# Kernel optimization log

Hardware: AMD Instinct MI355X
Metric: run time of the kernel (lower is better)

Reference implementation:

```python
import jax, jax.numpy as jnp
import numpy as np

N = 20000      # nodes (drugs, scaled to production size)
E = 640000     # edges
R = 65         # relation types
F_IN = 128     # input feature dim (trimnet embedding)
H1 = 64        # hidden1
H2 = 32        # hidden2 (bilinear discriminator dim)
B = 8192       # drug pairs in idx


def setup_inputs() -> dict:
    key = jax.random.key(0)
    ks = jax.random.split(key, 20)
    s = 0.05
    return {
        "x_o": jax.random.normal(ks[0], (N, F_IN), jnp.float32),
        "x_a": jax.random.normal(ks[1], (N, F_IN), jnp.float32),
        "features1": jax.random.normal(ks[2], (N, F_IN), jnp.float32),
        "W1": jax.random.normal(ks[3], (R, F_IN, H1), jnp.float32) * s,
        "root1": jax.random.normal(ks[4], (F_IN, H1), jnp.float32) * s,
        "b1": jnp.zeros((H1,), jnp.float32),
        "W2": jax.random.normal(ks[5], (R, H1, H2), jnp.float32) * s,
        "root2": jax.random.normal(ks[6], (H1, H2), jnp.float32) * s,
        "b2": jnp.zeros((H2,), jnp.float32),
        "attt": jnp.array([0.5, 0.5], jnp.float32),
        "disc_W": jax.random.normal(ks[7], (H2, H2), jnp.float32) * s,
        "disc_b": jnp.zeros((), jnp.float32),
        "cls_W": jax.random.normal(ks[8], (448, R), jnp.float32) * s,
        "cls_b": jnp.zeros((R,), jnp.float32),
        "edge_index": jax.random.randint(ks[9], (2, E), 0, N, jnp.int32),
        "e_type": jax.random.randint(ks[10], (E,), 0, R, jnp.int32),
        "e_type1": jax.random.randint(ks[11], (E,), 0, R, jnp.int32),
        "idx": jax.random.randint(ks[12], (2, B), 0, N, jnp.int32),
    }


def rgcn(x, src, dst, etype, W, root, b):
    """RGCNConv with per-relation mean aggregation (PyG default aggr='mean').
    Aggregates source features per (relation, dst) via one segment_sum, then
    applies the relation weights once with a batched matmul."""
    n, fin = x.shape
    seg = etype * n + dst                       # combined (relation, dst) segment id
    msg = x[src]                                # [E, fin] gather
    agg = jax.ops.segment_sum(msg, seg, num_segments=R * n).reshape(R, n, fin)
    cnt = jax.ops.segment_sum(jnp.ones((src.shape[0],), x.dtype), seg,
                              num_segments=R * n).reshape(R, n, 1)
    agg = agg / jnp.maximum(cnt, 1.0)           # per-relation mean
    out = jnp.einsum('rnf,rfh->nh', agg, W)     # sum over relations of W_r @ mean_r
    return out + x @ root + b


def reference(x_o, x_a, features1, W1, root1, b1, W2, root2, b2, attt,
              disc_W, disc_b, cls_W, cls_b, edge_index, e_type, e_type1, idx):
    src, dst = edge_index[0], edge_index[1]

    def enc(x, et):
        h1 = jax.nn.relu(rgcn(x, src, dst, et, W1, root1, b1))
        # dropout is identity in eval mode
        h2 = rgcn(h1, src, dst, et, W2, root2, b2)
        return h1, h2

    x1_o, x2_o = enc(x_o, e_type)
    _, x2_o_a = enc(x_a, e_type)
    _, x2_o_a_a = enc(x_o, e_type1)

    c = jax.nn.sigmoid(jnp.mean(x2_o, axis=0))  # readout + sigmoid, [H2]

    def disc(h_pl, h_mi):
        s1 = h_pl @ disc_W @ c + disc_b         # bilinear f_k(h, c)
        s2 = h_mi @ disc_W @ c + disc_b
        return jnp.stack([s1, s2], axis=1)      # [N, 2]

    ret_os = disc(x2_o, x2_o_a)
    ret_os_a = disc(x2_o, x2_o_a_a)

    final = jnp.concatenate([attt[0] * x1_o, attt[1] * x2_o], axis=1)  # [N, 96]
    e1 = jnp.concatenate([final[idx[0]], features1[idx[0]]], axis=1)   # [B, 224]
    e2 = jnp.concatenate([final[idx[1]], features1[idx[1]]], axis=1)
    log = jnp.concatenate([e1, e2], axis=1) @ cls_W + cls_b            # [B, 65]
    return (log, ret_os, ret_os_a, x2_o)
```

## Files before the change

kernel.cpp:

```cpp
#include <hip/hip_runtime.h>
#include <hip/hip_bf16.h>

#define NN 20000
#define EE 640000
#define RR 65
#define FIN1 128
#define HH1 64
#define HH2 32
#define BB 8192

constexpr int BM = 128;
constexpr int NBH = 256;
constexpr int GRID_PRE = 2048;
constexpr int EPB = EE / NBH;
constexpr int NBT = (NN + BM - 1) / BM;
constexpr int NOCT = 8;
constexpr int NPO = NN / NOCT;
constexpr int NB2 = NOCT * RR;
constexpr int MAXT2 = EE / BM + NB2;

constexpr int CLS_K  = 512;
constexpr int CLS_N  = 80;
constexpr int CLS_CK = 128;
constexpr int CLS_BM = 64;

typedef __attribute__((ext_vector_type(8))) short short8;
typedef __attribute__((ext_vector_type(4))) float floatx4;
typedef __attribute__((ext_vector_type(4))) unsigned int uint4e;
typedef __attribute__((ext_vector_type(2))) unsigned int uint2e;

constexpr size_t aln(size_t x) { return (x + 255) & ~(size_t)255; }

constexpr size_t OFF_CSUM  = 0;
constexpr size_t OFF_CNTD  = aln(OFF_CSUM + 32 * 4);
constexpr size_t ZERO_BYTES = OFF_CNTD + (size_t)NN * 4;
constexpr size_t OFF_DSTOFF = aln(ZERO_BYTES);
constexpr size_t OFF_BH0   = aln(OFF_DSTOFF + ((size_t)NN + 1) * 4);
constexpr size_t OFF_BH1   = OFF_BH0 + (size_t)NBH * NB2 * 4;
constexpr size_t OFF_BB0   = OFF_BH1 + (size_t)NBH * NB2 * 4;
constexpr size_t OFF_BB1   = OFF_BB0 + (size_t)NBH * NB2 * 4;
constexpr size_t OFF_HT    = aln(OFF_BB1 + (size_t)NBH * NB2 * 4);
constexpr size_t OFF_OFFB0 = aln(OFF_HT + (size_t)2 * NB2 * 4);
constexpr size_t OFF_OFFB1 = OFF_OFFB0 + (NB2 + 1) * 4;
constexpr size_t OFF_TILB0 = aln(OFF_OFFB1 + (NB2 + 1) * 4);
constexpr size_t OFF_TILT0 = OFF_TILB0 + (size_t)MAXT2 * 4;
constexpr size_t OFF_TILB1 = OFF_TILT0 + (size_t)MAXT2 * 4;
constexpr size_t OFF_TILT1 = OFF_TILB1 + (size_t)MAXT2 * 4;
constexpr size_t OFF_SLOT  = aln(OFF_TILT1 + (size_t)MAXT2 * 4);
constexpr size_t OFF_POSD  = OFF_SLOT + (size_t)EE * 4;
constexpr size_t OFF_RDP   = OFF_POSD + (size_t)EE * 4;
constexpr size_t OFF_WD0   = OFF_RDP + (size_t)EE * 4;
constexpr size_t OFF_WD1   = OFF_WD0 + (size_t)EE * 4;
constexpr size_t OFF_PERM0 = OFF_WD1 + (size_t)EE * 4;
constexpr size_t OFF_PERM1 = OFF_PERM0 + (size_t)EE * 4;
constexpr size_t OFF_XOB   = aln(OFF_PERM1 + (size_t)EE * 4);
constexpr size_t OFF_XAB   = OFF_XOB + (size_t)NN * FIN1 * 2;
constexpr size_t OFF_H1    = aln(OFF_XAB + (size_t)NN * FIN1 * 2);
constexpr size_t OFF_H1B   = OFF_H1 + (size_t)3 * NN * HH1 * 4;
constexpr size_t OFF_X2A   = OFF_H1B + (size_t)3 * NN * HH1 * 2;
constexpr size_t OFF_X2AA  = OFF_X2A + (size_t)NN * HH2 * 4;
constexpr size_t OFF_W1BT  = OFF_X2AA + (size_t)NN * HH2 * 4;
constexpr size_t OFF_W2BT  = OFF_W1BT + (size_t)RR * HH1 * FIN1 * 2;
constexpr size_t OFF_R1T   = OFF_W2BT + (size_t)RR * HH2 * HH1 * 2;
constexpr size_t OFF_R2T   = OFF_R1T + (size_t)HH1 * FIN1 * 2;
constexpr size_t OFF_CWT   = OFF_R2T + (size_t)HH2 * HH1 * 2;
constexpr size_t OFF_PART  = aln(OFF_CWT + (size_t)CLS_N * CLS_K * 2);
constexpr size_t OFF_MSG   = aln(OFF_PART + (size_t)256 * 32 * 4);
constexpr size_t MSG_B1    = (size_t)EE * HH1 * 2;
constexpr size_t MSG_B2    = (size_t)EE * HH2 * 2;
constexpr size_t WS_END    = OFF_MSG + MSG_B1;

constexpr size_t O_LOG  = 0;
constexpr size_t O_ROS  = (size_t)BB * RR;
constexpr size_t O_ROSA = O_ROS + (size_t)NN * 2;
constexpr size_t O_X2O  = O_ROSA + (size_t)NN * 2;

__device__ inline unsigned short f2bf(float f) {
    __hip_bfloat16 h = __float2bfloat16(f);
    return *reinterpret_cast<unsigned short*>(&h);
}
__device__ inline float bfbits2f(unsigned int hi_bits) {
    return __uint_as_float(hi_bits);
}

struct GemmEnc {
    const unsigned short* X;
    unsigned short* msg;
    const unsigned int* perm;
    const int* offB;
    const int* tilB;
    const int* tilT;
};
struct GemmArgs { GemmEnc e[3]; };

struct RedEnc {
    const unsigned short* msg;
    const float* wD;
    float* base;
    unsigned short* bfout;
};
struct RedArgs { RedEnc e[3]; };

__global__ void k_hist(const int* __restrict__ ei, const int* __restrict__ et0,
                       const int* __restrict__ et1,
                       int* cntD, int* __restrict__ slotE,
                       int* __restrict__ bh0, int* __restrict__ bh1,
                       const float* __restrict__ x_o, const float* __restrict__ x_a,
                       const float* __restrict__ W1, const float* __restrict__ W2,
                       const float* __restrict__ root1, const float* __restrict__ root2,
                       const float* __restrict__ clsW,
                       unsigned short* xob, unsigned short* xab,
                       unsigned short* w1t, unsigned short* w2t,
                       unsigned short* r1t, unsigned short* r2t,
                       unsigned short* cwt) {
    __shared__ int lh0[NB2], lh1[NB2];
    int t = threadIdx.x;
    if (blockIdx.x < NBH) {
        for (int p = t; p < NB2; p += 256) { lh0[p] = 0; lh1[p] = 0; }
        __syncthreads();
        int base = blockIdx.x * EPB;
        for (int i = t; i < EPB; i += 256) {
            int e = base + i;
            int oct = ei[e] / NPO;
            atomicAdd(&lh0[oct * RR + et0[e]], 1);
            atomicAdd(&lh1[oct * RR + et1[e]], 1);
            slotE[e] = atomicAdd(&cntD[ei[EE + e]], 1);
        }
        __syncthreads();
        for (int p = t; p < NB2; p += 256) {
            bh0[blockIdx.x * NB2 + p] = lh0[p];
            bh1[blockIdx.x * NB2 + p] = lh1[p];
        }
    }
    int stride = gridDim.x * 256;
    int i0 = blockIdx.x * 256 + t;
    const int NX4 = NN * FIN1 / 4;
    const float4* xo4 = (const float4*)x_o;
    const float4* xa4 = (const float4*)x_a;
    for (int i = i0; i < NX4; i += stride) {
        float4 a = xo4[i], b = xa4[i];
        uint2 pa, pb;
        pa.x = (unsigned)f2bf(a.x) | ((unsigned)f2bf(a.y) << 16);
        pa.y = (unsigned)f2bf(a.z) | ((unsigned)f2bf(a.w) << 16);
        pb.x = (unsigned)f2bf(b.x) | ((unsigned)f2bf(b.y) << 16);
        pb.y = (unsigned)f2bf(b.z) | ((unsigned)f2bf(b.w) << 16);
        ((uint2*)xob)[i] = pa;
        ((uint2*)xab)[i] = pb;
    }
    const int NW1_4 = RR * HH1 * FIN1 / 4;
    for (int i4 = i0; i4 < NW1_4; i4 += stride) {
        int i = i4 * 4;
        int k = i % FIN1; int rh = i / FIN1; int hh = rh % HH1; int r = rh / HH1;
        const float* s = &W1[((size_t)r * FIN1 + k) * HH1 + hh];
        uint2 pk;
        pk.x = (unsigned)f2bf(s[0]) | ((unsigned)f2bf(s[HH1]) << 16);
        pk.y = (unsigned)f2bf(s[2 * HH1]) | ((unsigned)f2bf(s[3 * HH1]) << 16);
        ((uint2*)w1t)[i4] = pk;
    }
    const int NW2_4 = RR * HH2 * HH1 / 4;
    for (int i4 = i0; i4 < NW2_4; i4 += stride) {
        int i = i4 * 4;
        int k = i % HH1; int rh = i / HH1; int hh = rh % HH2; int r = rh / HH2;
        const float* s = &W2[((size_t)r * HH1 + k) * HH2 + hh];
        uint2 pk;
        pk.x = (unsigned)f2bf(s[0]) | ((unsigned)f2bf(s[HH2]) << 16);
        pk.y = (unsigned)f2bf(s[2 * HH2]) | ((unsigned)f2bf(s[3 * HH2]) << 16);
        ((uint2*)w2t)[i4] = pk;
    }
    const int NR1_4 = HH1 * FIN1 / 4;
    for (int i4 = i0; i4 < NR1_4; i4 += stride) {
        int i = i4 * 4;
        int k = i % FIN1; int hh = i / FIN1;
        const float* s = &root1[(size_t)k * HH1 + hh];
        uint2 pk;
        pk.x = (unsigned)f2bf(s[0]) | ((unsigned)f2bf(s[HH1]) << 16);
        pk.y = (unsigned)f2bf(s[2 * HH1]) | ((unsigned)f2bf(s[3 * HH1]) << 16);
        ((uint2*)r1t)[i4] = pk;
    }
    const int NR2_4 = HH2 * HH1 / 4;
    for (int i4 = i0; i4 < NR2_4; i4 += stride) {
        int i = i4 * 4;
        int k = i % HH1; int hh = i / HH1;
        const float* s = &root2[(size_t)k * HH2 + hh];
        uint2 pk;
        pk.x = (unsigned)f2bf(s[0]) | ((unsigned)f2bf(s[HH2]) << 16);
        pk.y = (unsigned)f2bf(s[2 * HH2]) | ((unsigned)f2bf(s[3 * HH2]) << 16);
        ((uint2*)r2t)[i4] = pk;
    }
    const int NCW_4 = CLS_N * CLS_K / 4;
    for (int i4 = i0; i4 < NCW_4; i4 += stride) {
        int i = i4 * 4;
        int k = i % CLS_K; int n = i / CLS_K;
        uint2 pk = {0u, 0u};
        if (n < RR && k < 448) {
            const float* s = &clsW[(size_t)k * RR + n];
            pk.x = (unsigned)f2bf(s[0]) | ((unsigned)f2bf(s[RR]) << 16);
            pk.y = (unsigned)f2bf(s[2 * RR]) | ((unsigned)f2bf(s[3 * RR]) << 16);
        }
        ((uint2*)cwt)[i4] = pk;
    }
}

__global__ void k_scanD(const int* __restrict__ cntD, int* __restrict__ dstOff) {
    __shared__ int s[256];
    int t = threadIdx.x;
    constexpr int PER = (NN + 255) / 256;
    int lo = t * PER, hi = min(NN, lo + PER);
    int sum = 0;
    for (int i = lo; i < hi; i++) sum += cntD[i];
    s[t] = sum;
    __syncthreads();
    for (int ofs = 1; ofs < 256; ofs <<= 1) {
        int v = 0;
        if (t >= ofs) v = s[t - ofs];
        __syncthreads();
        if (t >= ofs) s[t] += v;
        __syncthreads();
    }
    int run = s[t] - sum;
    for (int i = lo; i < hi; i++) { dstOff[i] = run; run += cntD[i]; }
    if (t == 255) dstOff[NN] = run;
}

__global__ void k_post(const int* __restrict__ ei, const int* __restrict__ et0,
                       const int* __restrict__ et1, const int* __restrict__ dstOff,
                       const int* __restrict__ slotE,
                       int* __restrict__ posD, unsigned int* __restrict__ rdP) {
    int e = blockIdx.x * 256 + threadIdx.x;
    if (e < EE) {
        int d = ei[EE + e];
        int pos = dstOff[d] + slotE[e];
        posD[e] = pos;
        rdP[pos] = (unsigned)et0[e] | ((unsigned)et1[e] << 16);
    }
}

__global__ void k_scanB1(const int* __restrict__ bh0, const int* __restrict__ bh1,
                         int* __restrict__ bb0, int* __restrict__ bb1,
                         int* __restrict__ hT) {
    int w = (blockIdx.x * 256 + threadIdx.x) >> 6;
    int lane = threadIdx.x & 63;
    if (w >= 2 * NB2) return;
    int s = w / NB2, k = w % NB2;
    const int* bh = s ? bh1 : bh0;
    int* bb = s ? bb1 : bb0;
    int v[4];
    #pragma unroll
    for (int i = 0; i < 4; i++) v[i] = bh[(size_t)(lane * 4 + i) * NB2 + k];
    int ls = v[0] + v[1] + v[2] + v[3];
    int inc = ls;
    #pragma unroll
    for (int ofs = 1; ofs < 64; ofs <<= 1) {
        int o = __shfl_up(inc, ofs);
        if (lane >= ofs) inc += o;
    }
    int run = inc - ls;
    #pragma unroll
    for (int i = 0; i < 4; i++) {
        bb[(size_t)(lane * 4 + i) * NB2 + k] = run;
        run += v[i];
    }
    if (lane == 63) hT[s * NB2 + k] = run;
}

__global__ void k_scanB2(const int* __restrict__ hT,
                         int* offB0, int* offB1,
                         int* tilB0, int* tilT0, int* tilB1, int* tilT1) {
    __shared__ int h[2][NB2];
    __shared__ int o[2][NB2 + 1];
    __shared__ int to[2][NB2 + 1];
    __shared__ int csumE[2][8], csumT[2][8];
    int t = threadIdx.x;
    for (int p = t; p < 2 * NB2; p += 256) h[p / NB2][p % NB2] = hT[p];
    __syncthreads();
    if (t < 16) {
        int s = t / 8, c = t % 8;
        int runE = 0, runT = 0;
        for (int k = c * RR; k < (c + 1) * RR; k++) {
            o[s][k] = runE;  runE += h[s][k];
            to[s][k] = runT; runT += (h[s][k] + BM - 1) / BM;
        }
        csumE[s][c] = runE; csumT[s][c] = runT;
    }
    __syncthreads();
    if (t < 2) {
        int runE = 0, runT = 0;
        for (int c = 0; c < 8; c++) {
            int e = csumE[t][c], tt = csumT[t][c];
            csumE[t][c] = runE; csumT[t][c] = runT;
            runE += e; runT += tt;
        }
        o[t][NB2] = runE; to[t][NB2] = runT;
    }
    __syncthreads();
    if (t < 16) {
        int s = t / 8, c = t % 8;
        for (int k = c * RR; k < (c + 1) * RR; k++) {
            o[s][k] += csumE[s][c];
            to[s][k] += csumT[s][c];
        }
    }
    __syncthreads();
    for (int p = t; p <= NB2; p += 256) { offB0[p] = o[0][p]; offB1[p] = o[1][p]; }
    for (int i = t; i < MAXT2; i += 256) {
        #pragma unroll
        for (int s = 0; s < 2; s++) {
            int total = to[s][NB2];
            int bkt = -1, ti = 0;
            if (i < total) {
                int lo = 0, hi = NB2;
                while (hi - lo > 1) { int mid = (lo + hi) >> 1; if (to[s][mid] <= i) lo = mid; else hi = mid; }
                bkt = lo;
                ti = i - to[s][lo];
            }
            if (s == 0) { tilB0[i] = bkt; tilT0[i] = ti; }
            else        { tilB1[i] = bkt; tilT1[i] = ti; }
        }
    }
}

__global__ void k_fillB(const int* __restrict__ ei, const int* __restrict__ et0,
                        const int* __restrict__ et1, const int* __restrict__ posD,
                        const int* __restrict__ offB0, const int* __restrict__ offB1,
                        const int* __restrict__ bb0, const int* __restrict__ bb1,
                        unsigned int* perm0, unsigned int* perm1) {
    __shared__ int lc[2][NB2];
    __shared__ int lb[2][NB2];
    int t = threadIdx.x;
    for (int p = t; p < NB2; p += 256) {
        lc[0][p] = 0; lc[1][p] = 0;
        lb[0][p] = offB0[p] + bb0[blockIdx.x * NB2 + p];
        lb[1][p] = offB1[p] + bb1[blockIdx.x * NB2 + p];
    }
    __syncthreads();
    int base = blockIdx.x * EPB;
    for (int i = t; i < EPB; i += 256) {
        int e = base + i;
        int src = ei[e];
        int pos = posD[e];
        int oct = src / NPO;
        unsigned int packed = ((unsigned)(src - oct * NPO) << 20) | (unsigned)pos;
        int k0 = oct * RR + et0[e];
        int k1 = oct * RR + et1[e];
        int p0 = atomicAdd(&lc[0][k0], 1);
        int p1 = atomicAdd(&lc[1][k1], 1);
        perm0[lb[0][k0] + p0] = packed;
        perm1[lb[1][k1] + p1] = packed;
    }
}

__global__ void k_wts(const int* __restrict__ dstOff, const unsigned int* __restrict__ rdP,
                      float* __restrict__ wD0, float* __restrict__ wD1) {
    constexpr int CAP = 96;
    __shared__ unsigned int ld[4][CAP];
    int wave = threadIdx.x >> 6;
    int lane = threadIdx.x & 63;
    int d = blockIdx.x * 4 + wave;
    int j0 = 0, deg = 0;
    if (d < NN) { j0 = dstOff[d]; deg = dstOff[d + 1] - j0; }
    for (int j = lane; j < deg && j < CAP; j += 64) ld[wave][j] = rdP[j0 + j];
    __syncthreads();
    for (int j = lane; j < deg; j += 64) {
        unsigned int my = (j < CAP) ? ld[wave][j] : rdP[j0 + j];
        unsigned int m0 = my & 0xffffu, m1 = my >> 16;
        int c0 = 0, c1 = 0;
        for (int k = 0; k < deg; k++) {
            unsigned int p = (k < CAP) ? ld[wave][k] : rdP[j0 + k];
            c0 += ((p & 0xffffu) == m0);
            c1 += ((p >> 16) == m1);
        }
        wD0[j0 + j] = 1.0f / (float)c0;
        wD1[j0 + j] = 1.0f / (float)c1;
    }
}

template <int FIN, int HOUT>
__launch_bounds__(256, 3)
__global__ void k_bgemm(const unsigned short* __restrict__ X0,
                        const unsigned short* __restrict__ X1,
                        const unsigned short* __restrict__ X2,
                        const unsigned short* __restrict__ rootT,
                        const float* __restrict__ bias,
                        float* O0, float* O1, float* O2) {
    const int enc = blockIdx.y;
    const unsigned short* X = enc == 0 ? X0 : enc == 1 ? X1 : X2;
    float* O = enc == 0 ? O0 : enc == 1 ? O1 : O2;
    int n0 = blockIdx.x * BM;
    int mcount = min(BM, NN - n0);

    constexpr int LDK = FIN + 8;
    __shared__ unsigned short As[BM][LDK];
    __shared__ unsigned short Bs[HOUT][LDK];

    int tid = threadIdx.x;
    {
        constexpr int CHB = HOUT * FIN / 8;
        for (int c = tid; c < CHB; c += 256) {
            int row = c / (FIN / 8), cc = c % (FIN / 8);
            *(uint4*)&Bs[row][cc * 8] = *(const uint4*)&rootT[row * FIN + cc * 8];
        }
    }
    {
        constexpr int CHA = BM * FIN / 8;
        for (int c = tid; c < CHA; c += 256) {
            int row = c / (FIN / 8), cc = c % (FIN / 8);
            uint4 v = {0u, 0u, 0u, 0u};
            if (row < mcount) v = *(const uint4*)&X[(size_t)(n0 + row) * FIN + cc * 8];
            *(uint4*)&As[row][cc * 8] = v;
        }
    }
    __syncthreads();

    const int wave = tid >> 6;
    const int lane = tid & 63;
    const int q = lane >> 4;
    const int ln = lane & 15;
    constexpr int NT = HOUT / 16;
    constexpr int KS = FIN / 32;
    const int mbase = wave * 32;

    floatx4 acc[2][NT];
    #pragma unroll
    for (int a = 0; a < 2; a++)
        #pragma unroll
        for (int nt = 0; nt < NT; nt++) acc[a][nt] = floatx4{0.f, 0.f, 0.f, 0.f};

    for (int ks = 0; ks < KS; ks++) {
        int kk = ks * 32 + q * 8;
        short8 af0 = *(const short8*)&As[mbase + ln][kk];
        short8 af1 = *(const short8*)&As[mbase + 16 + ln][kk];
        #pragma unroll
        for (int nt = 0; nt < NT; nt++) {
            short8 bf = *(const short8*)&Bs[nt * 16 + ln][kk];
            acc[0][nt] = __builtin_amdgcn_mfma_f32_16x16x32_bf16(af0, bf, acc[0][nt], 0, 0, 0);
            acc[1][nt] = __builtin_amdgcn_mfma_f32_16x16x32_bf16(af1, bf, acc[1][nt], 0, 0, 0);
        }
    }

    #pragma unroll
    for (int mt = 0; mt < 2; mt++) {
        #pragma unroll
        for (int rr2 = 0; rr2 < 4; rr2++) {
            int i = mbase + mt * 16 + q * 4 + rr2;
            int n = n0 + i;
            if (i < mcount) {
                #pragma unroll
                for (int nt = 0; nt < NT; nt++)
                    O[(size_t)n * HOUT + nt * 16 + ln] = acc[mt][nt][rr2] + bias[nt * 16 + ln];
            }
        }
    }
}

template <int FIN, int HOUT>
__launch_bounds__(1024, 8)
__global__ void k_gemm(GemmArgs ga, const unsigned short* __restrict__ WT) {
    const GemmEnc ge = ga.e[blockIdx.y];
    int b = blockIdx.x;
    int bkt = ge.tilB[b];
    if (bkt < 0) return;
    int r = bkt % RR;
    int srcBase = (bkt / RR) * NPO;
    int t = ge.tilT[b];
    int ebase = ge.offB[bkt] + t * BM;
    int mcount = min(BM, ge.offB[bkt + 1] - ebase);

    constexpr int LDK = FIN + 8;
    __shared__ unsigned short As[BM][LDK];
    __shared__ unsigned short Bs[HOUT][LDK];
    __shared__ int Sr[BM];
    __shared__ int Pd[BM];

    int tid = threadIdx.x;
    if (tid < BM) {
        if (tid < mcount) {
            unsigned int p = ge.perm[ebase + tid];
            Sr[tid] = srcBase + (int)(p >> 20);
            Pd[tid] = (int)(p & 0xFFFFFu);
        } else { Sr[tid] = -1; Pd[tid] = 0; }
    }
    __syncthreads();

    {
        const unsigned short* Wr = WT + (size_t)r * HOUT * FIN;
        constexpr int CHB = HOUT * FIN / 8;
        for (int c = tid; c < CHB; c += 1024) {
            int row = c / (FIN / 8), cc = c % (FIN / 8);
            *(uint4*)&Bs[row][cc * 8] = *(const uint4*)&Wr[row * FIN + cc * 8];
        }
    }
    {
        constexpr int CHA = BM * FIN / 8;
        for (int c = tid; c < CHA; c += 1024) {
            int row = c / (FIN / 8), cc = c % (FIN / 8);
            int s = Sr[row];
            uint4 v = {0u, 0u, 0u, 0u};
            if (s >= 0) v = *(const uint4*)&ge.X[(size_t)s * FIN + cc * 8];
            *(uint4*)&As[row][cc * 8] = v;
        }
    }
    __syncthreads();

    const int wave = tid >> 6;
    const int lane = tid & 63;
    const int q = lane >> 4;
    const int ln = lane & 15;
    constexpr int NT = HOUT / 32;
    constexpr int KS = FIN / 32;
    const int mbase = (wave & 7) * 16;
    const int nbase = (wave >> 3) * (HOUT / 2);

    floatx4 acc[NT];
    #pragma unroll
    for (int nt = 0; nt < NT; nt++) acc[nt] = floatx4{0.f, 0.f, 0.f, 0.f};

    #pragma unroll
    for (int ks = 0; ks < KS; ks++) {
        int kk = ks * 32 + q * 8;
        short8 af = *(const short8*)&As[mbase + ln][kk];
        #pragma unroll
        for (int nt = 0; nt < NT; nt++) {
            short8 bf = *(const short8*)&Bs[nbase + nt * 16 + ln][kk];
            acc[nt] = __builtin_amdgcn_mfma_f32_16x16x32_bf16(af, bf, acc[nt], 0, 0, 0);
        }
    }

    #pragma unroll
    for (int rr2 = 0; rr2 < 4; rr2++) {
        int i = mbase + q * 4 + rr2;
        if (i < mcount) {
            unsigned short* mrow = ge.msg + (size_t)Pd[i] * HOUT + nbase + ln;
            #pragma unroll
            for (int nt = 0; nt < NT; nt++)
                mrow[nt * 16] = f2bf(acc[nt][rr2]);
        }
    }
}

template <int H, bool RELU>
__global__ void k_reduce(RedArgs ra, const int* __restrict__ dstOff) {
    const RedEnc re = ra.e[blockIdx.y];
    int d = blockIdx.x * 4 + (threadIdx.x >> 6);
    if (d >= NN) return;
    int lane = threadIdx.x & 63;
    constexpr int HC = H / 4;
    constexpr int RPI = 64 / HC;
    int sub = lane / HC;
    int c4 = lane % HC;
    int j0 = dstOff[d], j1 = dstOff[d + 1];
    double a0 = 0.0, a1 = 0.0, a2 = 0.0, a3 = 0.0;
    for (int j = j0 + sub; j < j1; j += RPI) {
        float w = re.wD[j];
        uint2e v = *(const uint2e*)&re.msg[(size_t)j * H + c4 * 4];
        a0 += (double)(w * bfbits2f(v.x << 16));
        a1 += (double)(w * bfbits2f(v.x & 0xffff0000u));
        a2 += (double)(w * bfbits2f(v.y << 16));
        a3 += (double)(w * bfbits2f(v.y & 0xffff0000u));
    }
    #pragma unroll
    for (int ofs = 32; ofs >= HC; ofs >>= 1) {
        a0 += __shfl_down(a0, ofs); a1 += __shfl_down(a1, ofs);
        a2 += __shfl_down(a2, ofs); a3 += __shfl_down(a3, ofs);
    }
    if (lane < HC) {
        size_t o = (size_t)d * H + c4 * 4;
        float v0 = re.base[o] + (float)a0, v1 = re.base[o + 1] + (float)a1;
        float v2 = re.base[o + 2] + (float)a2, v3 = re.base[o + 3] + (float)a3;
        if (RELU) {
            v0 = fmaxf(v0, 0.f); v1 = fmaxf(v1, 0.f);
            v2 = fmaxf(v2, 0.f); v3 = fmaxf(v3, 0.f);
        }
        re.base[o] = v0; re.base[o + 1] = v1; re.base[o + 2] = v2; re.base[o + 3] = v3;
        if (RELU) {
            re.bfout[o] = f2bf(v0); re.bfout[o + 1] = f2bf(v1);
            re.bfout[o + 2] = f2bf(v2); re.bfout[o + 3] = f2bf(v3);
        }
    }
}

__global__ void k_mean(const float* __restrict__ x2o, float* __restrict__ part) {
    __shared__ float s[256];
    int t = threadIdx.x; int hh = t & 31; int g = t >> 5;
    float acc = 0.f;
    for (int n = blockIdx.x * 8 + g; n < NN; n += gridDim.x * 8)
        acc += x2o[(size_t)n * 32 + hh];
    s[t] = acc;
    __syncthreads();
    if (t < 32) {
        float v = 0.f;
        for (int gg = 0; gg < 8; gg++) v += s[gg * 32 + t];
        part[blockIdx.x * 32 + t] = v;
    }
}

__global__ void k_csum(const float* __restrict__ part, float* __restrict__ csum) {
    int t = threadIdx.x;
    if (t < 32) {
        double a = 0.0;
        for (int b = 0; b < 256; b++) a += (double)part[b * 32 + t];
        csum[t] = (float)a;
    }
}

__global__ void k_disc(const float* __restrict__ x2o, const float* __restrict__ x2a,
                       const float* __restrict__ x2aa, const float* __restrict__ csum,
                       const float* __restrict__ discW, const float* __restrict__ discb,
                       float* ret_os, float* ret_osa) {
    __shared__ float c[32], v[32];
    int t = threadIdx.x;
    if (t < 32) c[t] = 1.f / (1.f + expf(-csum[t] * (1.f / NN)));
    __syncthreads();
    if (t < 32) {
        float a = 0.f;
        for (int j = 0; j < 32; j++) a += discW[t * 32 + j] * c[j];
        v[t] = a;
    }
    __syncthreads();
    float db = discb[0];
    int n = blockIdx.x * 256 + t;
    if (n < NN) {
        float s1 = 0.f, s2 = 0.f, s3 = 0.f;
        for (int j = 0; j < 32; j++) {
            float vj = v[j];
            s1 += x2o[(size_t)n * 32 + j] * vj;
            s2 += x2a[(size_t)n * 32 + j] * vj;
            s3 += x2aa[(size_t)n * 32 + j] * vj;
        }
        ret_os[n * 2] = s1 + db;  ret_os[n * 2 + 1] = s2 + db;
        ret_osa[n * 2] = s1 + db; ret_osa[n * 2 + 1] = s3 + db;
    }
}

__launch_bounds__(256, 2)
__global__ void k_clsg(const float* __restrict__ h1o, const float* __restrict__ x2o,
                       const float* __restrict__ feat, const float* __restrict__ attt,
                       const int* __restrict__ idx,
                       const unsigned short* __restrict__ cwt,
                       const float* __restrict__ clsb, float* __restrict__ log_out) {
    constexpr int LDK = CLS_CK + 8;
    __shared__ unsigned short As[CLS_BM][LDK];
    __shared__ unsigned short Bs[CLS_N][LDK];
    __shared__ int nd[2][CLS_BM];

    int tid = threadIdx.x;
    int p0 = blockIdx.x * CLS_BM;
    if (tid < CLS_BM) {
        nd[0][tid] = idx[p0 + tid];
        nd[1][tid] = idx[BB + p0 + tid];
    }
    float a0 = attt[0], a1 = attt[1];

    const int wave = tid >> 6;
    const int lane = tid & 63;
    const int q = lane >> 4;
    const int ln = lane & 15;
    constexpr int NT = CLS_N / 16;
    const int mbase = wave * 16;

    floatx4 acc[NT];
    #pragma unroll
    for (int nt = 0; nt < NT; nt++) acc[nt] = floatx4{0.f, 0.f, 0.f, 0.f};

    for (int ch = 0; ch < CLS_K / CLS_CK; ch++) {
        int kbase = ch * CLS_CK;
        __syncthreads();
        for (int c = tid; c < CLS_N * CLS_CK / 8; c += 256) {
            int row = c / (CLS_CK / 8), cc = c % (CLS_CK / 8);
            *(uint4*)&Bs[row][cc * 8] = *(const uint4*)&cwt[(size_t)row * CLS_K + kbase + cc * 8];
        }
        for (int c = tid; c < CLS_BM * CLS_CK / 4; c += 256) {
            int row = c / (CLS_CK / 4);
            int j4 = (c % (CLS_CK / 4)) * 4;
            int j = kbase + j4;
            float4 v = {0.f, 0.f, 0.f, 0.f};
            if (j < 448) {
                int hseg = j / 224, jj = j % 224;
                int node = nd[hseg][row];
                if (jj < 64) {
                    v = *(const float4*)&h1o[(size_t)node * 64 + jj];
                    v.x *= a0; v.y *= a0; v.z *= a0; v.w *= a0;
                } else if (jj < 96) {
                    v = *(const float4*)&x2o[(size_t)node * 32 + (jj - 64)];
                    v.x *= a1; v.y *= a1; v.z *= a1; v.w *= a1;
                } else {
                    v = *(const float4*)&feat[(size_t)node * 128 + (jj - 96)];
                }
            }
            uint2 pk;
            pk.x = (unsigned)f2bf(v.x) | ((unsigned)f2bf(v.y) << 16);
            pk.y = (unsigned)f2bf(v.z) | ((unsigned)f2bf(v.w) << 16);
            *(uint2*)&As[row][j4] = pk;
        }
        __syncthreads();
        #pragma unroll
        for (int ks = 0; ks < CLS_CK / 32; ks++) {
            int kk = ks * 32 + q * 8;
            short8 af = *(const short8*)&As[mbase + ln][kk];
            #pragma unroll
            for (int nt = 0; nt < NT; nt++) {
                short8 bf = *(const short8*)&Bs[nt * 16 + ln][kk];
                acc[nt] = __builtin_amdgcn_mfma_f32_16x16x32_bf16(af, bf, acc[nt], 0, 0, 0);
            }
        }
    }

    #pragma unroll
    for (int rr2 = 0; rr2 < 4; rr2++) {
        int i = mbase + q * 4 + rr2;
        int pair = p0 + i;
        #pragma unroll
        for (int nt = 0; nt < NT; nt++) {
            int col = nt * 16 + ln;
            if (col < RR)
                log_out[(size_t)pair * RR + col] = acc[nt][rr2] + clsb[col];
        }
    }
}

extern "C" void kernel_launch(void* const* d_in, const int* in_sizes, int n_in,
                              void* d_out, int out_size, void* d_ws, size_t ws_size,
                              hipStream_t stream) {
    const float* x_o   = (const float*)d_in[0];
    const float* x_a   = (const float*)d_in[1];
    const float* feat  = (const float*)d_in[2];
    const float* W1    = (const float*)d_in[3];
    const float* root1 = (const float*)d_in[4];
    const float* b1    = (const float*)d_in[5];
    const float* W2    = (const float*)d_in[6];
    const float* root2 = (const float*)d_in[7];
    const float* b2    = (const float*)d_in[8];
    const float* attt  = (const float*)d_in[9];
    const float* discW = (const float*)d_in[10];
    const float* discb = (const float*)d_in[11];
    const float* clsW  = (const float*)d_in[12];
    const float* clsb  = (const float*)d_in[13];
    const int* ei      = (const int*)d_in[14];
    const int* et0     = (const int*)d_in[15];
    const int* et1     = (const int*)d_in[16];
    const int* idx     = (const int*)d_in[17];

    char* ws = (char*)d_ws;
    float* csum = (float*)(ws + OFF_CSUM);
    int* cntD  = (int*)(ws + OFF_CNTD);
    int* dstOff = (int*)(ws + OFF_DSTOFF);
    int* bh0   = (int*)(ws + OFF_BH0);
    int* bh1   = (int*)(ws + OFF_BH1);
    int* bb0   = (int*)(ws + OFF_BB0);
    int* bb1   = (int*)(ws + OFF_BB1);
    int* hT    = (int*)(ws + OFF_HT);
    int* offB0 = (int*)(ws + OFF_OFFB0);
    int* offB1 = (int*)(ws + OFF_OFFB1);
    int* tilB0 = (int*)(ws + OFF_TILB0);
    int* tilT0 = (int*)(ws + OFF_TILT0);
    int* tilB1 = (int*)(ws + OFF_TILB1);
    int* tilT1 = (int*)(ws + OFF_TILT1);
    int* slotE = (int*)(ws + OFF_SLOT);
    int* posD  = (int*)(ws + OFF_POSD);
    unsigned int* rdP = (unsigned int*)(ws + OFF_RDP);
    float* wD0 = (float*)(ws + OFF_WD0);
    float* wD1 = (float*)(ws + OFF_WD1);
    unsigned int* perm0 = (unsigned int*)(ws + OFF_PERM0);
    unsigned int* perm1 = (unsigned int*)(ws + OFF_PERM1);
    unsigned short* xob = (unsigned short*)(ws + OFF_XOB);
    unsigned short* xab = (unsigned short*)(ws + OFF_XAB);
    float* h1o  = (float*)(ws + OFF_H1);
    float* h1a  = h1o + (size_t)NN * HH1;
    float* h1aa = h1a + (size_t)NN * HH1;
    unsigned short* h1bo  = (unsigned short*)(ws + OFF_H1B);
    unsigned short* h1ba  = h1bo + (size_t)NN * HH1;
    unsigned short* h1baa = h1ba + (size_t)NN * HH1;
    float* x2a  = (float*)(ws + OFF_X2A);
    float* x2aa = (float*)(ws + OFF_X2AA);
    unsigned short* w1t = (unsigned short*)(ws + OFF_W1BT);
    unsigned short* w2t = (unsigned short*)(ws + OFF_W2BT);
    unsigned short* r1t = (unsigned short*)(ws + OFF_R1T);
    unsigned short* r2t = (unsigned short*)(ws + OFF_R2T);
    unsigned short* cwt = (unsigned short*)(ws + OFF_CWT);
    float* part = (float*)(ws + OFF_PART);
    unsigned short* msg = (unsigned short*)(ws + OFF_MSG);

    float* out = (float*)d_out;
    float* log_out = out + O_LOG;
    float* ret_os  = out + O_ROS;
    float* ret_osa = out + O_ROSA;
    float* x2o     = out + O_X2O;

    size_t availMsg = ws_size > OFF_MSG ? ws_size - OFF_MSG : MSG_B1;
    int nb1 = (availMsg >= 2 * MSG_B1) ? 2 : 1;
    int nb2 = (availMsg >= 3 * MSG_B2) ? 3 : (availMsg >= 2 * MSG_B2 ? 2 : 1);

    hipMemsetAsync(ws, 0, ZERO_BYTES, stream);

    k_hist<<<GRID_PRE, 256, 0, stream>>>(ei, et0, et1, cntD, slotE, bh0, bh1,
                                         x_o, x_a, W1, W2, root1, root2, clsW,
                                         xob, xab, w1t, w2t, r1t, r2t, cwt);
    k_scanD<<<1, 256, 0, stream>>>(cntD, dstOff);
    k_post<<<2500, 256, 0, stream>>>(ei, et0, et1, dstOff, slotE, posD, rdP);
    k_scanB1<<<(2 * NB2 + 3) / 4, 256, 0, stream>>>(bh0, bh1, bb0, bb1, hT);
    k_scanB2<<<1, 256, 0, stream>>>(hT, offB0, offB1,
                                    tilB0, tilT0, tilB1, tilT1);
    k_fillB<<<NBH, 256, 0, stream>>>(ei, et0, et1, posD, offB0, offB1, bb0, bb1,
                                     perm0, perm1);
    k_wts<<<NN / 4, 256, 0, stream>>>(dstOff, rdP, wD0, wD1);

    {
        dim3 gb(NBT, 3);
        k_bgemm<FIN1, HH1><<<gb, 256, 0, stream>>>(xob, xab, xob, r1t, b1,
                                                   h1o, h1a, h1aa);
        const unsigned short* Xs[3] = {xob, xab, xob};
        float* Os[3] = {h1o, h1a, h1aa};
        unsigned short* Obs[3] = {h1bo, h1ba, h1baa};
        for (int e0 = 0; e0 < 3; ) {
            int g = 3 - e0 < nb1 ? 3 - e0 : nb1;
            GemmArgs ga{};
            RedArgs ra{};
            for (int j = 0; j < g; j++) {
                int enc = e0 + j;
                unsigned short* mb = msg + (size_t)j * EE * HH1;
                ga.e[j].X    = Xs[enc];
                ga.e[j].msg  = mb;
                ga.e[j].perm = enc == 2 ? perm1 : perm0;
                ga.e[j].offB = enc == 2 ? offB1 : offB0;
                ga.e[j].tilB = enc == 2 ? tilB1 : tilB0;
                ga.e[j].tilT = enc == 2 ? tilT1 : tilT0;
                ra.e[j].msg  = mb;
                ra.e[j].wD   = enc == 2 ? wD1 : wD0;
                ra.e[j].base = Os[enc];
                ra.e[j].bfout = Obs[enc];
            }
            k_gemm<FIN1, HH1><<<dim3(MAXT2, g), 1024, 0, stream>>>(ga, w1t);
            k_reduce<HH1, true><<<dim3(NN / 4, g), 256, 0, stream>>>(ra, dstOff);
            e0 += g;
        }
    }

    {
        dim3 gb(NBT, 3);
        k_bgemm<HH1, HH2><<<gb, 256, 0, stream>>>(h1bo, h1ba, h1baa, r2t, b2,
                                                  x2o, x2a, x2aa);
        const unsigned short* Xs[3] = {h1bo, h1ba, h1baa};
        float* Os[3] = {x2o, x2a, x2aa};
        for (int e0 = 0; e0 < 3; ) {
            int g = 3 - e0 < nb2 ? 3 - e0 : nb2;
            GemmArgs ga{};
            RedArgs ra{};
            for (int j = 0; j < g; j++) {
                int enc = e0 + j;
                unsigned short* mb = msg + (size_t)j * EE * HH2;
                ga.e[j].X    = Xs[enc];
                ga.e[j].msg  = mb;
                ga.e[j].perm = enc == 2 ? perm1 : perm0;
                ga.e[j].offB = enc == 2 ? offB1 : offB0;
                ga.e[j].tilB = enc == 2 ? tilB1 : tilB0;
                ga.e[j].tilT = enc == 2 ? tilT1 : tilT0;
                ra.e[j].msg  = mb;
                ra.e[j].wD   = enc == 2 ? wD1 : wD0;
                ra.e[j].base = Os[enc];
                ra.e[j].bfout = nullptr;
            }
            k_gemm<HH1, HH2><<<dim3(MAXT2, g), 1024, 0, stream>>>(ga, w2t);
            k_reduce<HH2, false><<<dim3(NN / 4, g), 256, 0, stream>>>(ra, dstOff);
            e0 += g;
        }
    }

    k_mean<<<256, 256, 0, stream>>>(x2o, part);
    k_csum<<<1, 64, 0, stream>>>(part, csum);
    k_disc<<<(NN + 255) / 256, 256, 0, stream>>>(x2o, x2a, x2aa, csum, discW, discb,
                                                 ret_os, ret_osa);
    k_clsg<<<BB / CLS_BM, 256, 0, stream>>>(h1o, x2o, feat, attt, idx, cwt, clsb, log_out);
}
```

Baseline: 613.4 us.

## Fuse per-edge message reduction into GEMM via fixed-point integer atomics

Rather than writing bf16 per-edge messages to a buffer and reducing them per destination in a separate kernel, the GEMM now scales each result by the edge weight, converts it to 20-bit fixed point and atomically adds it into a per-node int accumulator. Lightweight finish kernels add the accumulator to the root-term output, applying ReLU and bf16 conversion for layer 1. All three encoders run in one launch and the block becomes 512 threads, with each wave covering all output columns. This removes the large message buffer traffic and the reduce launches. It adds heavy int atomic contention and a fixed-point range and precision limit. Integer atomics keep the sum deterministic.

Result: slower. 837.9 us (+36.6%).

```diff
diff --git a/kernel.cpp b/kernel.cpp
--- a/kernel.cpp
+++ b/kernel.cpp
@@ -24,10 +24,11 @@
 constexpr int CLS_CK = 128;
 constexpr int CLS_BM = 64;
 
+constexpr float FXS  = 1048576.0f;
+constexpr float FXSI = 1.0f / 1048576.0f;
+
 typedef __attribute__((ext_vector_type(8))) short short8;
 typedef __attribute__((ext_vector_type(4))) float floatx4;
-typedef __attribute__((ext_vector_type(4))) unsigned int uint4e;
-typedef __attribute__((ext_vector_type(2))) unsigned int uint2e;
 
 constexpr size_t aln(size_t x) { return (x + 255) & ~(size_t)255; }
 
@@ -65,10 +66,10 @@
 constexpr size_t OFF_R2T   = OFF_R1T + (size_t)HH1 * FIN1 * 2;
 constexpr size_t OFF_CWT   = OFF_R2T + (size_t)HH2 * HH1 * 2;
 constexpr size_t OFF_PART  = aln(OFF_CWT + (size_t)CLS_N * CLS_K * 2);
-constexpr size_t OFF_MSG   = aln(OFF_PART + (size_t)256 * 32 * 4);
-constexpr size_t MSG_B1    = (size_t)EE * HH1 * 2;
-constexpr size_t MSG_B2    = (size_t)EE * HH2 * 2;
-constexpr size_t WS_END    = OFF_MSG + MSG_B1;
+constexpr size_t OFF_ACC1  = aln(OFF_PART + (size_t)256 * 32 * 4);
+constexpr size_t OFF_ACC2  = OFF_ACC1 + (size_t)3 * NN * HH1 * 4;
+constexpr size_t OFF_DSTP  = OFF_ACC2 + (size_t)3 * NN * HH2 * 4;
+constexpr size_t ACC_ZB    = (size_t)3 * NN * (HH1 + HH2) * 4;
 
 constexpr size_t O_LOG  = 0;
 constexpr size_t O_ROS  = (size_t)BB * RR;
@@ -79,27 +80,19 @@
     __hip_bfloat16 h = __float2bfloat16(f);
     return *reinterpret_cast<unsigned short*>(&h);
 }
-__device__ inline float bfbits2f(unsigned int hi_bits) {
-    return __uint_as_float(hi_bits);
-}
 
 struct GemmEnc {
     const unsigned short* X;
-    unsigned short* msg;
+    int* acc;
     const unsigned int* perm;
     const int* offB;
     const int* tilB;
     const int* tilT;
+    const float* wD;
 };
 struct GemmArgs { GemmEnc e[3]; };
 
-struct RedEnc {
-    const unsigned short* msg;
-    const float* wD;
-    float* base;
-    unsigned short* bfout;
-};
-struct RedArgs { RedEnc e[3]; };
+struct Fin2P { float* o[3]; };
 
 __global__ void k_hist(const int* __restrict__ ei, const int* __restrict__ et0,
                        const int* __restrict__ et1,
@@ -225,13 +218,15 @@
 __global__ void k_post(const int* __restrict__ ei, const int* __restrict__ et0,
                        const int* __restrict__ et1, const int* __restrict__ dstOff,
                        const int* __restrict__ slotE,
-                       int* __restrict__ posD, unsigned int* __restrict__ rdP) {
+                       int* __restrict__ posD, unsigned int* __restrict__ rdP,
+                       int* __restrict__ dstP) {
     int e = blockIdx.x * 256 + threadIdx.x;
     if (e < EE) {
         int d = ei[EE + e];
         int pos = dstOff[d] + slotE[e];
         posD[e] = pos;
         rdP[pos] = (unsigned)et0[e] | ((unsigned)et1[e] << 16);
+        dstP[pos] = d;
     }
 }
 
@@ -453,8 +448,9 @@
 }
 
 template <int FIN, int HOUT>
-__launch_bounds__(1024, 8)
-__global__ void k_gemm(GemmArgs ga, const unsigned short* __restrict__ WT) {
+__launch_bounds__(512, 6)
+__global__ void k_gemm(GemmArgs ga, const unsigned short* __restrict__ WT,
+                       const int* __restrict__ dstP) {
     const GemmEnc ge = ga.e[blockIdx.y];
     int b = blockIdx.x;
     int bkt = ge.tilB[b];
@@ -469,29 +465,32 @@
     __shared__ unsigned short As[BM][LDK];
     __shared__ unsigned short Bs[HOUT][LDK];
     __shared__ int Sr[BM];
-    __shared__ int Pd[BM];
+    __shared__ int Dd[BM];
+    __shared__ float Wt[BM];
 
     int tid = threadIdx.x;
     if (tid < BM) {
         if (tid < mcount) {
             unsigned int p = ge.perm[ebase + tid];
+            int pos = (int)(p & 0xFFFFFu);
             Sr[tid] = srcBase + (int)(p >> 20);
-            Pd[tid] = (int)(p & 0xFFFFFu);
-        } else { Sr[tid] = -1; Pd[tid] = 0; }
+            Dd[tid] = dstP[pos];
+            Wt[tid] = ge.wD[pos];
+        } else { Sr[tid] = -1; Dd[tid] = 0; Wt[tid] = 0.f; }
     }
     __syncthreads();
 
     {
         const unsigned short* Wr = WT + (size_t)r * HOUT * FIN;
         constexpr int CHB = HOUT * FIN / 8;
-        for (int c = tid; c < CHB; c += 1024) {
+        for (int c = tid; c < CHB; c += 512) {
             int row = c / (FIN / 8), cc = c % (FIN / 8);
             *(uint4*)&Bs[row][cc * 8] = *(const uint4*)&Wr[row * FIN + cc * 8];
         }
     }
     {
         constexpr int CHA = BM * FIN / 8;
-        for (int c = tid; c < CHA; c += 1024) {
+        for (int c = tid; c < CHA; c += 512) {
             int row = c / (FIN / 8), cc = c % (FIN / 8);
             int s = Sr[row];
             uint4 v = {0u, 0u, 0u, 0u};
@@ -505,10 +504,9 @@
     const int lane = tid & 63;
     const int q = lane >> 4;
     const int ln = lane & 15;
-    constexpr int NT = HOUT / 32;
+    constexpr int NT = HOUT / 16;
     constexpr int KS = FIN / 32;
-    const int mbase = (wave & 7) * 16;
-    const int nbase = (wave >> 3) * (HOUT / 2);
+    const int mbase = wave * 16;
 
     floatx4 acc[NT];
     #pragma unroll
@@ -520,7 +518,7 @@
         short8 af = *(const short8*)&As[mbase + ln][kk];
         #pragma unroll
         for (int nt = 0; nt < NT; nt++) {
-            short8 bf = *(const short8*)&Bs[nbase + nt * 16 + ln][kk];
+            short8 bf = *(const short8*)&Bs[nt * 16 + ln][kk];
             acc[nt] = __builtin_amdgcn_mfma_f32_16x16x32_bf16(af, bf, acc[nt], 0, 0, 0);
         }
     }
@@ -529,52 +527,50 @@
     for (int rr2 = 0; rr2 < 4; rr2++) {
         int i = mbase + q * 4 + rr2;
         if (i < mcount) {
-            unsigned short* mrow = ge.msg + (size_t)Pd[i] * HOUT + nbase + ln;
+            float w = Wt[i];
+            int* arow = ge.acc + (size_t)Dd[i] * HOUT + ln;
             #pragma unroll
-            for (int nt = 0; nt < NT; nt++)
-                mrow[nt * 16] = f2bf(acc[nt][rr2]);
-        }
-    }
-}
-
-template <int H, bool RELU>
-__global__ void k_reduce(RedArgs ra, const int* __restrict__ dstOff) {
-    const RedEnc re = ra.e[blockIdx.y];
-    int d = blockIdx.x * 4 + (threadIdx.x >> 6);
-    if (d >= NN) return;
-    int lane = threadIdx.x & 63;
-    constexpr int HC = H / 4;
-    constexpr int RPI = 64 / HC;
-    int sub = lane / HC;
-    int c4 = lane % HC;
-    int j0 = dstOff[d], j1 = dstOff[d + 1];
-    double a0 = 0.0, a1 = 0.0, a2 = 0.0, a3 = 0.0;
-    for (int j = j0 + sub; j < j1; j += RPI) {
-        float w = re.wD[j];
-        uint2e v = *(const uint2e*)&re.msg[(size_t)j * H + c4 * 4];
-        a0 += (double)(w * bfbits2f(v.x << 16));
-        a1 += (double)(w * bfbits2f(v.x & 0xffff0000u));
-        a2 += (double)(w * bfbits2f(v.y << 16));
-        a3 += (double)(w * bfbits2f(v.y & 0xffff0000u));
-    }
-    #pragma unroll
-    for (int ofs = 32; ofs >= HC; ofs >>= 1) {
-        a0 += __shfl_down(a0, ofs); a1 += __shfl_down(a1, ofs);
-        a2 += __shfl_down(a2, ofs); a3 += __shfl_down(a3, ofs);
-    }
-    if (lane < HC) {
-        size_t o = (size_t)d * H + c4 * 4;
-        float v0 = re.base[o] + (float)a0, v1 = re.base[o + 1] + (float)a1;
-        float v2 = re.base[o + 2] + (float)a2, v3 = re.base[o + 3] + (float)a3;
-        if (RELU) {
-            v0 = fmaxf(v0, 0.f); v1 = fmaxf(v1, 0.f);
-            v2 = fmaxf(v2, 0.f); v3 = fmaxf(v3, 0.f);
-        }
-        re.base[o] = v0; re.base[o + 1] = v1; re.base[o + 2] = v2; re.base[o + 3] = v3;
-        if (RELU) {
-            re.bfout[o] = f2bf(v0); re.bfout[o + 1] = f2bf(v1);
-            re.bfout[o + 2] = f2bf(v2); re.bfout[o + 3] = f2bf(v3);
-        }
+            for (int nt = 0; nt < NT; nt++) {
+                int fx = __float2int_rn(w * acc[nt][rr2] * FXS);
+                atomicAdd(arow + nt * 16, fx);
+            }
+        }
+    }
+}
+
+__global__ void k_fin1(float* __restrict__ h, const int* __restrict__ acc,
+                       unsigned short* __restrict__ hb) {
+    int i = blockIdx.x * 256 + threadIdx.x;
+    const int N4 = 3 * NN * HH1 / 4;
+    if (i < N4) {
+        float4 b = ((const float4*)h)[i];
+        int4 a = ((const int4*)acc)[i];
+        float v0 = fmaxf(b.x + (float)a.x * FXSI, 0.f);
+        float v1 = fmaxf(b.y + (float)a.y * FXSI, 0.f);
+        float v2 = fmaxf(b.z + (float)a.z * FXSI, 0.f);
+        float v3 = fmaxf(b.w + (float)a.w * FXSI, 0.f);
+        ((float4*)h)[i] = float4{v0, v1, v2, v3};
+        uint2 pk;
+        pk.x = (unsigned)f2bf(v0) | ((unsigned)f2bf(v1) << 16);
+        pk.y = (unsigned)f2bf(v2) | ((unsigned)f2bf(v3) << 16);
+        ((uint2*)hb)[i] = pk;
+    }
+}
+
+__global__ void k_fin2(Fin2P fp, const int* __restrict__ acc) {
+    int enc = blockIdx.y;
+    float* o = fp.o[enc];
+    const int* a = acc + (size_t)enc * NN * HH2;
+    int i = blockIdx.x * 256 + threadIdx.x;
+    const int N4 = NN * HH2 / 4;
+    if (i < N4) {
+        float4 b = ((const float4*)o)[i];
+        int4 v = ((const int4*)a)[i];
+        b.x += (float)v.x * FXSI;
+        b.y += (float)v.y * FXSI;
+        b.z += (float)v.z * FXSI;
+        b.w += (float)v.w * FXSI;
+        ((float4*)o)[i] = b;
     }
 }
 
@@ -777,7 +773,9 @@
     unsigned short* r2t = (unsigned short*)(ws + OFF_R2T);
     unsigned short* cwt = (unsigned short*)(ws + OFF_CWT);
     float* part = (float*)(ws + OFF_PART);
-    unsigned short* msg = (unsigned short*)(ws + OFF_MSG);
+    int* acc1  = (int*)(ws + OFF_ACC1);
+    int* acc2  = (int*)(ws + OFF_ACC2);
+    int* dstP  = (int*)(ws + OFF_DSTP);
 
     float* out = (float*)d_out;
     float* log_out = out + O_LOG;
@@ -785,17 +783,14 @@
     float* ret_osa = out + O_ROSA;
     float* x2o     = out + O_X2O;
 
-    size_t availMsg = ws_size > OFF_MSG ? ws_size - OFF_MSG : MSG_B1;
-    int nb1 = (availMsg >= 2 * MSG_B1) ? 2 : 1;
-    int nb2 = (availMsg >= 3 * MSG_B2) ? 3 : (availMsg >= 2 * MSG_B2 ? 2 : 1);
-
     hipMemsetAsync(ws, 0, ZERO_BYTES, stream);
+    hipMemsetAsync(ws + OFF_ACC1, 0, ACC_ZB, stream);
 
     k_hist<<<GRID_PRE, 256, 0, stream>>>(ei, et0, et1, cntD, slotE, bh0, bh1,
                                          x_o, x_a, W1, W2, root1, root2, clsW,
                                          xob, xab, w1t, w2t, r1t, r2t, cwt);
     k_scanD<<<1, 256, 0, stream>>>(cntD, dstOff);
-    k_post<<<2500, 256, 0, stream>>>(ei, et0, et1, dstOff, slotE, posD, rdP);
+    k_post<<<2500, 256, 0, stream>>>(ei, et0, et1, dstOff, slotE, posD, rdP, dstP);
     k_scanB1<<<(2 * NB2 + 3) / 4, 256, 0, stream>>>(bh0, bh1, bb0, bb1, hT);
     k_scanB2<<<1, 256, 0, stream>>>(hT, offB0, offB1,
                                     tilB0, tilT0, tilB1, tilT1);
@@ -808,30 +803,18 @@
         k_bgemm<FIN1, HH1><<<gb, 256, 0, stream>>>(xob, xab, xob, r1t, b1,
                                                    h1o, h1a, h1aa);
         const unsigned short* Xs[3] = {xob, xab, xob};
-        float* Os[3] = {h1o, h1a, h1aa};
-        unsigned short* Obs[3] = {h1bo, h1ba, h1baa};
-        for (int e0 = 0; e0 < 3; ) {
-            int g = 3 - e0 < nb1 ? 3 - e0 : nb1;
-            GemmArgs ga{};
-            RedArgs ra{};
-            for (int j = 0; j < g; j++) {
-                int enc = e0 + j;
-                unsigned short* mb = msg + (size_t)j * EE * HH1;
-                ga.e[j].X    = Xs[enc];
-                ga.e[j].msg  = mb;
-                ga.e[j].perm = enc == 2 ? perm1 : perm0;
-                ga.e[j].offB = enc == 2 ? offB1 : offB0;
-                ga.e[j].tilB = enc == 2 ? tilB1 : tilB0;
-                ga.e[j].tilT = enc == 2 ? tilT1 : tilT0;
-                ra.e[j].msg  = mb;
-                ra.e[j].wD   = enc == 2 ? wD1 : wD0;
-                ra.e[j].base = Os[enc];
-                ra.e[j].bfout = Obs[enc];
-            }
-            k_gemm<FIN1, HH1><<<dim3(MAXT2, g), 1024, 0, stream>>>(ga, w1t);
-            k_reduce<HH1, true><<<dim3(NN / 4, g), 256, 0, stream>>>(ra, dstOff);
-            e0 += g;
-        }
+        GemmArgs ga{};
+        for (int enc = 0; enc < 3; enc++) {
+            ga.e[enc].X    = Xs[enc];
+            ga.e[enc].acc  = acc1 + (size_t)enc * NN * HH1;
+            ga.e[enc].perm = enc == 2 ? perm1 : perm0;
+            ga.e[enc].offB = enc == 2 ? offB1 : offB0;
+            ga.e[enc].tilB = enc == 2 ? tilB1 : tilB0;
+            ga.e[enc].tilT = enc == 2 ? tilT1 : tilT0;
+            ga.e[enc].wD   = enc == 2 ? wD1 : wD0;
+        }
+        k_gemm<FIN1, HH1><<<dim3(MAXT2, 3), 512, 0, stream>>>(ga, w1t, dstP);
+        k_fin1<<<(3 * NN * HH1 / 4 + 255) / 256, 256, 0, stream>>>(h1o, acc1, h1bo);
     }
 
     {
@@ -839,29 +822,20 @@
         k_bgemm<HH1, HH2><<<gb, 256, 0, stream>>>(h1bo, h1ba, h1baa, r2t, b2,
                                                   x2o, x2a, x2aa);
         const unsigned short* Xs[3] = {h1bo, h1ba, h1baa};
-        float* Os[3] = {x2o, x2a, x2aa};
-        for (int e0 = 0; e0 < 3; ) {
-            int g = 3 - e0 < nb2 ? 3 - e0 : nb2;
-            GemmArgs ga{};
-            RedArgs ra{};
-            for (int j = 0; j < g; j++) {
-                int enc = e0 + j;
-                unsigned short* mb = msg + (size_t)j * EE * HH2;
-                ga.e[j].X    = Xs[enc];
-                ga.e[j].msg  = mb;
-                ga.e[j].perm = enc == 2 ? perm1 : perm0;
-                ga.e[j].offB = enc == 2 ? offB1 : offB0;
-                ga.e[j].tilB = enc == 2 ? tilB1 : tilB0;
-                ga.e[j].tilT = enc == 2 ? tilT1 : tilT0;
-                ra.e[j].msg  = mb;
-                ra.e[j].wD   = enc == 2 ? wD1 : wD0;
-                ra.e[j].base = Os[enc];
-                ra.e[j].bfout = nullptr;
-            }
-            k_gemm<HH1, HH2><<<dim3(MAXT2, g), 1024, 0, stream>>>(ga, w2t);
-            k_reduce<HH2, false><<<dim3(NN / 4, g), 256, 0, stream>>>(ra, dstOff);
-            e0 += g;
-        }
+        GemmArgs ga{};
+        for (int enc = 0; enc < 3; enc++) {
+            ga.e[enc].X    = Xs[enc];
+            ga.e[enc].acc  = acc2 + (size_t)enc * NN * HH2;
+            ga.e[enc].perm = enc == 2 ? perm1 : perm0;
+            ga.e[enc].offB = enc == 2 ? offB1 : offB0;
+            ga.e[enc].tilB = enc == 2 ? tilB1 : tilB0;
+            ga.e[enc].tilT = enc == 2 ? tilT1 : tilT0;
+            ga.e[enc].wD   = enc == 2 ? wD1 : wD0;
+        }
+        k_gemm<HH1, HH2><<<dim3(MAXT2, 3), 512, 0, stream>>>(ga, w2t, dstP);
+        Fin2P fp;
+        fp.o[0] = x2o; fp.o[1] = x2a; fp.o[2] = x2aa;
+        k_fin2<<<dim3(NN * HH2 / 4 / 256 + 1, 3), 256, 0, stream>>>(fp, acc2);
     }
 
     k_mean<<<256, 256, 0, stream>>>(x2o, part);
```
